# Kernel optimization log

Measured on AMD Instinct MI355X. Metric: run time of the kernel, lower is better.

Reference implementation:

```python
import jax, jax.numpy as jnp
import numpy as np

EPS = 1e-5

def _layernorm(x, g, b):
    m = jnp.mean(x, axis=-1, keepdims=True)
    v = jnp.mean(jnp.square(x - m), axis=-1, keepdims=True)
    return (x - m) * jax.lax.rsqrt(v + EPS) * g + b

def setup_inputs() -> dict:
    key = jax.random.key(0)
    B, S, D, H = 2, 2048, 1024, 16
    F = 4 * D
    ks = jax.random.split(key, 12)
    s = 1.0 / np.sqrt(D)
    inp = {
        "x": jax.random.normal(ks[0], (B, S, D), dtype=jnp.float32),
        "mask": jnp.ones((B, S), dtype=jnp.int32),
        "wq": jax.random.normal(ks[1], (D, D), dtype=jnp.float32) * s,
        "bq": jnp.zeros((D,), jnp.float32),
        "wk": jax.random.normal(ks[2], (D, D), dtype=jnp.float32) * s,
        "bk": jnp.zeros((D,), jnp.float32),
        "wv": jax.random.normal(ks[3], (D, D), dtype=jnp.float32) * s,
        "bv": jnp.zeros((D,), jnp.float32),
        "wo": jax.random.normal(ks[4], (D, D), dtype=jnp.float32) * s,
        "bo": jnp.zeros((D,), jnp.float32),
        "g1": jnp.ones((D,), jnp.float32),
        "be1": jnp.zeros((D,), jnp.float32),
        "g2": jnp.ones((D,), jnp.float32),
        "be2": jnp.zeros((D,), jnp.float32),
        "w1": jax.random.normal(ks[5], (D, F), dtype=jnp.float32) * s,
        "bf1": jnp.zeros((F,), jnp.float32),
        "w2": jax.random.normal(ks[6], (F, D), dtype=jnp.float32) * (1.0 / np.sqrt(F)),
        "bf2": jnp.zeros((D,), jnp.float32),
    }
    return inp

def reference(x, mask, wq, bq, wk, bk, wv, bv, wo, bo, g1, be1, g2, be2, w1, bf1, w2, bf2):
    B, S, D = x.shape
    H = 16
    hd = D // H
    residual = x
    xn = _layernorm(x, g1, be1)
    q = (xn @ wq + bq).reshape(B, S, H, hd).transpose(0, 2, 1, 3)  # [B,H,S,hd]
    k = (xn @ wk + bk).reshape(B, S, H, hd).transpose(0, 2, 1, 3)
    v = (xn @ wv + bv).reshape(B, S, H, hd).transpose(0, 2, 1, 3)
    scores = jnp.einsum('bhqd,bhkd->bhqk', q, k) / np.sqrt(hd)  # [B,H,S,S]
    scores = jnp.where(mask[:, None, None, :] == 0, jnp.float32(-1e9), scores)
    attn = jax.nn.softmax(scores, axis=-1)
    attended = jnp.einsum('bhqk,bhkd->bhqd', attn, v)
    attended = attended.transpose(0, 2, 1, 3).reshape(B, S, D)
    x = residual + (attended @ wo + bo)
    residual = x
    xn = _layernorm(x, g2, be2)
    ff = jax.nn.relu(xn @ w1 + bf1) @ w2 + bf2
    return residual + ff
```

## Files before the change

### kernel.cpp

```cpp
#include <hip/hip_runtime.h>
#include <hip/hip_bf16.h>


using bf16 = __hip_bfloat16;
typedef short bf16x8 __attribute__((ext_vector_type(8)));
typedef short bf16x4v __attribute__((ext_vector_type(4)));
typedef float f32x4 __attribute__((ext_vector_type(4)));

#if defined(__has_builtin)
#  if __has_builtin(__builtin_amdgcn_mfma_f32_16x16x16bf16_1k)
#    define HAVE_MFMA_K16 1
#  endif
#  if __has_builtin(__builtin_amdgcn_exp2f)
#    define EXP2F(x) __builtin_amdgcn_exp2f(x)
#  endif
#endif
#ifndef EXP2F
#  define EXP2F(x) __expf(0.6931471805599453f * (x))
#endif

__device__ __forceinline__ float toF(float v) { return v; }
__device__ __forceinline__ float toF(bf16 v) { return __bfloat162float(v); }
__device__ __forceinline__ void storeF(float* p, float v) { *p = v; }
__device__ __forceinline__ void storeF(bf16* p, float v) { *p = __float2bfloat16(v); }

__device__ __forceinline__ float waveReduceSum(float v) {
    #pragma unroll
    for (int o = 32; o > 0; o >>= 1) v += __shfl_down(v, o, 64);
    return v;
}

__device__ __forceinline__ void async16(const bf16* g, bf16* l) {
    __builtin_amdgcn_global_load_lds(
        (const __attribute__((address_space(1))) unsigned int*)g,
        (__attribute__((address_space(3))) unsigned int*)l,
        16, 0, 0);
}

__device__ __forceinline__ unsigned short bf16bits(float x) {
    union { bf16 h; unsigned short u; } e; e.h = __float2bfloat16(x);
    return e.u;
}

__global__ __launch_bounds__(256) void transpose_all(
        const float* __restrict__ wq, const float* __restrict__ wk,
        const float* __restrict__ wv, const float* __restrict__ wo,
        const float* __restrict__ w1, const float* __restrict__ w2,
        bf16* __restrict__ wqkvT, bf16* __restrict__ woT,
        bf16* __restrict__ w1T, bf16* __restrict__ w2T) {
    __shared__ float t[32][33];
    const int tI = blockIdx.x;
    const float* in; bf16* outT; int R, C, tl;
    if (tI < 4096) {
        const int seg = tI >> 10; tl = tI & 1023; R = 1024; C = 1024;
        in = (seg == 0) ? wq : (seg == 1) ? wk : (seg == 2) ? wv : wo;
        outT = (seg == 3) ? woT : wqkvT + (size_t)seg * 1024 * 1024;
    } else if (tI < 8192) {
        tl = tI - 4096; in = w1; outT = w1T; R = 1024; C = 4096;
    } else {
        tl = tI - 8192; in = w2; outT = w2T; R = 4096; C = 1024;
    }
    const int tc = C >> 5;
    const int c0 = (tl % tc) * 32, r0 = (tl / tc) * 32;
    const int lx = threadIdx.x & 31, ly = threadIdx.x >> 5;
    #pragma unroll
    for (int i = 0; i < 32; i += 8)
        t[ly + i][lx] = in[(size_t)(r0 + ly + i) * C + c0 + lx];
    __syncthreads();
    #pragma unroll
    for (int i = 0; i < 32; i += 8)
        outT[(size_t)(c0 + ly + i) * R + r0 + lx] = __float2bfloat16(t[lx][ly + i]);
}

template <typename InT>
__global__ __launch_bounds__(256) void ln_kernel(const InT* __restrict__ x,
                                                 const float* __restrict__ g,
                                                 const float* __restrict__ b,
                                                 bf16* __restrict__ out, int D) {
    const int row = blockIdx.x;
    const InT* xr = x + (size_t)row * D;
    float s = 0.f, s2 = 0.f;
    for (int i = threadIdx.x; i < D; i += 256) {
        float v = toF(xr[i]);
        s += v; s2 += v * v;
    }
    __shared__ float ws[4], ws2[4];
    int lane = threadIdx.x & 63, wid = threadIdx.x >> 6;
    s = waveReduceSum(s); s2 = waveReduceSum(s2);
    if (lane == 0) { ws[wid] = s; ws2[wid] = s2; }
    __syncthreads();
    float ts = ws[0] + ws[1] + ws[2] + ws[3];
    float ts2 = ws2[0] + ws2[1] + ws2[2] + ws2[3];
    float mean = ts / D;
    float var = ts2 / D - mean * mean;
    float rstd = rsqrtf(var + 1e-5f);
    bf16* outr = out + (size_t)row * D;
    for (int i = threadIdx.x; i < D; i += 256) {
        float v = (toF(xr[i]) - mean) * rstd * g[i] + b[i];
        outr[i] = __float2bfloat16(v);
    }
}

template <int BM, typename OutT, typename ResidT, bool RELU, bool HAS_RESID, bool BIAS3>
__global__ __launch_bounds__(256) void gemm_mfma(const bf16* __restrict__ A,
                                                 const bf16* __restrict__ BT,
                                                 const float* __restrict__ bias,
                                                 const float* __restrict__ biasK,
                                                 const float* __restrict__ biasV,
                                                 const ResidT* __restrict__ resid,
                                                 OutT* __restrict__ C,
                                                 int M, int N, int K) {
    constexpr int BK = 64;
    constexpr int MI = BM / 32;
    constexpr int AROWS = BM / 4;
    constexpr int ASEC = AROWS / 8;
    __shared__ bf16 As[BM][BK];
    __shared__ bf16 Bs[128][BK];
    const int tid = threadIdx.x, lane = tid & 63, wid = tid >> 6;
    const int m0 = blockIdx.y * BM, n0 = blockIdx.x * 128;
    const int wm = (BM == 128) ? (wid >> 1) * 64 : (wid & 1) * 32;
    const int wn = (BM == 128) ? (wid & 1) * 64 : (wid >> 1) * 64;

    f32x4 acc[MI][4] = {};

    const int srow = lane >> 3;
    const int scol = ((lane & 7) ^ srow) * 8;
    const bf16* Abase = A + (size_t)(m0 + wid * AROWS + srow) * K + scol;
    const bf16* Bbase = BT + (size_t)(n0 + wid * 32 + srow) * K + scol;

    const int fr = lane & 15;
    const int kg = lane >> 4;

    for (int k0 = 0; k0 < K; k0 += BK) {
        #pragma unroll
        for (int s = 0; s < ASEC; ++s)
            async16(Abase + (size_t)(s * 8) * K + k0, &As[wid * AROWS + s * 8][0]);
        #pragma unroll
        for (int s = 0; s < 4; ++s)
            async16(Bbase + (size_t)(s * 8) * K + k0, &Bs[wid * 32 + s * 8][0]);
        __syncthreads();

        #pragma unroll
        for (int ks = 0; ks < 2; ++ks) {
            const int pc = ((ks * 4 + kg) ^ (fr & 7)) * 16;
            bf16x8 aF[MI], bF[4];
            #pragma unroll
            for (int i = 0; i < MI; ++i)
                aF[i] = *(const bf16x8*)((const char*)&As[0][0]
                         + (size_t)(wm + i * 16 + fr) * 128 + pc);
            #pragma unroll
            for (int j = 0; j < 4; ++j)
                bF[j] = *(const bf16x8*)((const char*)&Bs[0][0]
                         + (size_t)(wn + j * 16 + fr) * 128 + pc);
            #pragma unroll
            for (int i = 0; i < MI; ++i)
                #pragma unroll
                for (int j = 0; j < 4; ++j)
                    acc[i][j] = __builtin_amdgcn_mfma_f32_16x16x32_bf16(
                        aF[i], bF[j], acc[i][j], 0, 0, 0);
        }
        __syncthreads();
    }

    const int col_l = lane & 15, row_l = (lane >> 4) * 4;
    #pragma unroll
    for (int j = 0; j < 4; ++j) {
        const int col = n0 + wn + j * 16 + col_l;
        float bvv;
        if (BIAS3) {
            const float* bp = (col < 1024) ? bias : ((col < 2048) ? biasK : biasV);
            bvv = bp[col & 1023];
        } else {
            bvv = bias[col];
        }
        #pragma unroll
        for (int i = 0; i < MI; ++i) {
            #pragma unroll
            for (int r = 0; r < 4; ++r) {
                const int row = m0 + wm + i * 16 + row_l + r;
                float v = acc[i][j][r] + bvv;
                if (RELU) v = fmaxf(v, 0.f);
                if (HAS_RESID) v += toF(resid[(size_t)row * N + col]);
                storeF(&C[(size_t)row * N + col], v);
            }
        }
    }
}

#if HAVE_MFMA_K16
__global__ __launch_bounds__(256) void attn_mfma(const bf16* __restrict__ qkv,
                                                 const int* __restrict__ mask,
                                                 bf16* __restrict__ outp,
                                                 int B, int S, int LD) {
    const int q0 = blockIdx.x * 128;
    const int h = blockIdx.y, b = blockIdx.z;
    const int Do = 1024;
    const int tid = threadIdx.x, lane = tid & 63, wid = tid >> 6;
    const int n = lane & 15, kg = lane >> 4;

    __shared__ bf16 Ks[64][66];
    __shared__ bf16 Vt[64][68];
    __shared__ float Mskf[64];

    const float QSCALE = 0.125f * 1.4426950408889634f;
    bf16x8 qf[2][2];
    #pragma unroll
    for (int u = 0; u < 2; ++u) {
        const bf16* qp = qkv + ((size_t)(b * S + q0 + wid * 32 + u * 16 + n)) * LD + h * 64 + kg * 8;
        union { uint4 uu; bf16x8 v; unsigned short s[8]; } c[2];
        c[0].uu = *(const uint4*)qp;
        c[1].uu = *(const uint4*)(qp + 32);
        #pragma unroll
        for (int t = 0; t < 2; ++t) {
            #pragma unroll
            for (int i = 0; i < 8; ++i) {
                union { float f; unsigned int u2; } d;
                d.u2 = ((unsigned int)c[t].s[i]) << 16;
                c[t].s[i] = bf16bits(d.f * QSCALE);
            }
            qf[u][t] = c[t].v;
        }
    }

    f32x4 acc[2][4] = {};
    float m[2] = {-1e30f, -1e30f}, l[2] = {0.f, 0.f};

    const int sr = tid >> 2, sc = (tid & 3) * 16;
    const int jp = tid & 31, dg = (tid >> 5) * 8;
    const bf16* kbase = qkv + (size_t)(b * S) * LD + 1024 + h * 64;
    const bf16* vbase = qkv + (size_t)(b * S) * LD + 2048 + h * 64;

    for (int j0 = 0; j0 < S; j0 += 64) {
        __syncthreads();
        {
            const bf16* kp = kbase + (size_t)(j0 + sr) * LD + sc;
            uint4 ka = *(const uint4*)kp;
            uint4 kc = *(const uint4*)(kp + 8);
            uint* kd = (uint*)((char*)&Ks[0][0] + sr * 132 + sc * 2);
            kd[0] = ka.x; kd[1] = ka.y; kd[2] = ka.z; kd[3] = ka.w;
            kd[4] = kc.x; kd[5] = kc.y; kd[6] = kc.z; kd[7] = kc.w;

            const bf16* vp = vbase + (size_t)(j0 + 2 * jp) * LD + dg;
            union { uint4 u; unsigned short s[8]; } va, vc;
            va.u = *(const uint4*)vp;
            vc.u = *(const uint4*)(vp + LD);
            #pragma unroll
            for (int i = 0; i < 8; ++i) {
                unsigned int pk = (unsigned int)va.s[i] | ((unsigned int)vc.s[i] << 16);
                *(unsigned int*)((char*)&Vt[0][0] + (size_t)(dg + i) * 136 + jp * 4) = pk;
            }
            if (tid < 64) Mskf[tid] = (mask[b * S + j0 + tid] == 0) ? -1e9f : 0.f;
        }
        __syncthreads();

        f32x4 st[2][4] = {};
        #pragma unroll
        for (int ks = 0; ks < 2; ++ks) {
            #pragma unroll
            for (int jt = 0; jt < 4; ++jt) {
                union { uint u[4]; bf16x8 v; } kf;
                const uint* bp = (const uint*)((const char*)&Ks[0][0]
                                 + (size_t)(jt * 16 + n) * 132 + ks * 64 + kg * 16);
                kf.u[0] = bp[0]; kf.u[1] = bp[1]; kf.u[2] = bp[2]; kf.u[3] = bp[3];
                st[0][jt] = __builtin_amdgcn_mfma_f32_16x16x32_bf16(kf.v, qf[0][ks], st[0][jt], 0, 0, 0);
                st[1][jt] = __builtin_amdgcn_mfma_f32_16x16x32_bf16(kf.v, qf[1][ks], st[1][jt], 0, 0, 0);
            }
        }

        bf16x4v pf[2][4];
        #pragma unroll
        for (int u = 0; u < 2; ++u) {
            float mx = m[u];
            #pragma unroll
            for (int jt = 0; jt < 4; ++jt) {
                f32x4 mb = *(const f32x4*)&Mskf[jt * 16 + kg * 4];
                #pragma unroll
                for (int r = 0; r < 4; ++r) {
                    st[u][jt][r] += mb[r];
                    mx = fmaxf(mx, st[u][jt][r]);
                }
            }
            mx = fmaxf(mx, __shfl_xor(mx, 16, 64));
            mx = fmaxf(mx, __shfl_xor(mx, 32, 64));
            float alpha = EXP2F(m[u] - mx);
            m[u] = mx;
            float ls = 0.f;
            #pragma unroll
            for (int jt = 0; jt < 4; ++jt) {
                union { unsigned short s[4]; bf16x4v v; } pk;
                #pragma unroll
                for (int r = 0; r < 4; ++r) {
                    union { float f; unsigned int u2; } p;
                    p.f = EXP2F(st[u][jt][r] - mx);
                    p.u2 &= 0xffff0000u;
                    ls += p.f;
                    pk.s[r] = (unsigned short)(p.u2 >> 16);
                }
                pf[u][jt] = pk.v;
            }
            ls += __shfl_xor(ls, 16, 64);
            ls += __shfl_xor(ls, 32, 64);
            l[u] = l[u] * alpha + ls;
            #pragma unroll
            for (int dt = 0; dt < 4; ++dt)
                #pragma unroll
                for (int r = 0; r < 4; ++r) acc[u][dt][r] *= alpha;
        }

        #pragma unroll
        for (int jt = 0; jt < 4; ++jt) {
            #pragma unroll
            for (int dt = 0; dt < 4; ++dt) {
                union { uint u[2]; bf16x4v v; } vf;
                const uint* vpp = (const uint*)((const char*)&Vt[0][0]
                                  + (size_t)(dt * 16 + n) * 136 + jt * 32 + kg * 8);
                vf.u[0] = vpp[0]; vf.u[1] = vpp[1];
                acc[0][dt] = __builtin_amdgcn_mfma_f32_16x16x16bf16_1k(vf.v, pf[0][jt], acc[0][dt], 0, 0, 0);
                acc[1][dt] = __builtin_amdgcn_mfma_f32_16x16x16bf16_1k(vf.v, pf[1][jt], acc[1][dt], 0, 0, 0);
            }
        }
    }

    #pragma unroll
    for (int u = 0; u < 2; ++u) {
        float inv = (l[u] > 0.f) ? (1.f / l[u]) : 0.f;
        bf16* op = outp + ((size_t)(b * S + q0 + wid * 32 + u * 16 + n)) * Do + h * 64;
        #pragma unroll
        for (int dt = 0; dt < 4; ++dt) {
            union { unsigned short s[4]; uint2 u2; } w;
            #pragma unroll
            for (int r = 0; r < 4; ++r) w.s[r] = bf16bits(acc[u][dt][r] * inv);
            *(uint2*)(op + dt * 16 + kg * 4) = w.u2;
        }
    }
}
#else
__global__ __launch_bounds__(256) void attn_mfma(const bf16* __restrict__ qkv,
                                                 const int* __restrict__ mask,
                                                 bf16* __restrict__ outp,
                                                 int B, int S, int LD) {
    const int h = blockIdx.y, b = blockIdx.z;
    const int Do = 1024;
    const int tid = threadIdx.x, lane = tid & 63, wid = tid >> 6;
    const int n = lane & 15, kg = lane >> 4;

    __shared__ bf16 Ks[64][66];
    __shared__ bf16 Vt[64][66];
    __shared__ bf16 Plds[4][16][66];
    __shared__ int  Msk[64];

    for (int half = 0; half < 2; ++half) {
        const int q0 = blockIdx.x * 128 + half * 64;
        __syncthreads();

        bf16x8 qf[2];
        {
            const bf16* qp = qkv + ((size_t)(b * S + q0 + wid * 16 + n)) * LD + h * 64 + kg * 8;
            union { uint4 u; bf16x8 v; } c0, c1;
            c0.u = *(const uint4*)qp;
            c1.u = *(const uint4*)(qp + 32);
            qf[0] = c0.v; qf[1] = c1.v;
        }

        f32x4 acc_o[4] = {};
        float m_r[4] = {-1e30f, -1e30f, -1e30f, -1e30f};
        float l_r[4] = {0.f, 0.f, 0.f, 0.f};

        const int sr = tid >> 2;
        const int sc = (tid & 3) * 16;
        const bf16* kbase = qkv + (size_t)(b * S) * LD + 1024 + h * 64;
        const bf16* vbase = qkv + (size_t)(b * S) * LD + 2048 + h * 64;

        for (int j0 = 0; j0 < S; j0 += 64) {
            __syncthreads();
            {
                const bf16* kp = kbase + (size_t)(j0 + sr) * LD + sc;
                uint4 ka = *(const uint4*)kp;
                uint4 kbv = *(const uint4*)(kp + 8);
                uint* kd = (uint*)((char*)&Ks[0][0] + sr * 132 + sc * 2);
                kd[0] = ka.x; kd[1] = ka.y; kd[2] = ka.z; kd[3] = ka.w;
                kd[4] = kbv.x; kd[5] = kbv.y; kd[6] = kbv.z; kd[7] = kbv.w;

                const bf16* vp = vbase + (size_t)(j0 + sr) * LD + sc;
                union { uint4 u[2]; unsigned short s[16]; } vv;
                vv.u[0] = *(const uint4*)vp;
                vv.u[1] = *(const uint4*)(vp + 8);
                #pragma unroll
                for (int i = 0; i < 16; ++i)
                    *((unsigned short*)((char*)&Vt[0][0] + (size_t)(sc + i) * 132 + sr * 2)) = vv.s[i];

                if (tid < 64) Msk[tid] = mask[b * S + j0 + tid];
            }
            __syncthreads();

            f32x4 st[4] = {};
            #pragma unroll
            for (int ks = 0; ks < 2; ++ks) {
                #pragma unroll
                for (int jt = 0; jt < 4; ++jt) {
                    union { uint u[4]; bf16x8 v; } bf;
                    const uint* bp = (const uint*)((const char*)&Ks[0][0]
                                     + (size_t)(jt * 16 + n) * 132 + ks * 64 + kg * 16);
                    bf.u[0] = bp[0]; bf.u[1] = bp[1]; bf.u[2] = bp[2]; bf.u[3] = bp[3];
                    st[jt] = __builtin_amdgcn_mfma_f32_16x16x32_bf16(qf[ks], bf.v, st[jt], 0, 0, 0);
                }
            }

            int mk[4];
            #pragma unroll
            for (int jt = 0; jt < 4; ++jt) mk[jt] = Msk[jt * 16 + n];

            #pragma unroll
            for (int r = 0; r < 4; ++r) {
                float mx = -1e30f;
                #pragma unroll
                for (int jt = 0; jt < 4; ++jt) {
                    float s = st[jt][r] * 0.125f;
                    if (mk[jt] == 0) s = -1e9f;
                    st[jt][r] = s;
                    mx = fmaxf(mx, s);
                }
                #pragma unroll
                for (int o = 1; o < 16; o <<= 1) mx = fmaxf(mx, __shfl_xor(mx, o, 64));
                float newm = fmaxf(m_r[r], mx);
                float alpha = __expf(m_r[r] - newm);
                m_r[r] = newm;
                float ls = 0.f;
                #pragma unroll
                for (int jt = 0; jt < 4; ++jt) {
                    float p = __expf(st[jt][r] - newm);
                    ls += p;
                    Plds[wid][kg * 4 + r][jt * 16 + n] = __float2bfloat16(p);
                }
                #pragma unroll
                for (int o = 1; o < 16; o <<= 1) ls += __shfl_xor(ls, o, 64);
                l_r[r] = l_r[r] * alpha + ls;
                #pragma unroll
                for (int dt = 0; dt < 4; ++dt) acc_o[dt][r] *= alpha;
            }

            __asm__ volatile("s_waitcnt lgkmcnt(0)" ::: "memory");

            #pragma unroll
            for (int ks = 0; ks < 2; ++ks) {
                union { uint u[4]; bf16x8 v; } af;
                const uint* ap = (const uint*)((const char*)&Plds[wid][0][0]
                                 + (size_t)n * 132 + ks * 64 + kg * 16);
                af.u[0] = ap[0]; af.u[1] = ap[1]; af.u[2] = ap[2]; af.u[3] = ap[3];
                #pragma unroll
                for (int dt = 0; dt < 4; ++dt) {
                    union { uint u[4]; bf16x8 v; } bf;
                    const uint* bp = (const uint*)((const char*)&Vt[0][0]
                                     + (size_t)(dt * 16 + n) * 132 + ks * 64 + kg * 16);
                    bf.u[0] = bp[0]; bf.u[1] = bp[1]; bf.u[2] = bp[2]; bf.u[3] = bp[3];
                    acc_o[dt] = __builtin_amdgcn_mfma_f32_16x16x32_bf16(af.v, bf.v, acc_o[dt], 0, 0, 0);
                }
            }
        }

        #pragma unroll
        for (int r = 0; r < 4; ++r) {
            float inv = (l_r[r] > 0.f) ? (1.f / l_r[r]) : 0.f;
            bf16* op = outp + ((size_t)(b * S + q0 + wid * 16 + kg * 4 + r)) * Do + h * 64 + n;
            #pragma unroll
            for (int dt = 0; dt < 4; ++dt)
                op[dt * 16] = __float2bfloat16(acc_o[dt][r] * inv);
        }
    }
}
#endif

extern "C" void kernel_launch(void* const* d_in, const int* in_sizes, int n_in,
                              void* d_out, int out_size, void* d_ws, size_t ws_size,
                              hipStream_t stream) {
    const int B = 2, S = 2048, D = 1024, H = 16, F = 4096;
    const int M = B * S;

    const float* x   = (const float*)d_in[0];
    const int*   mask= (const int*)  d_in[1];
    const float* wq  = (const float*)d_in[2];
    const float* bq  = (const float*)d_in[3];
    const float* wk  = (const float*)d_in[4];
    const float* bk  = (const float*)d_in[5];
    const float* wv  = (const float*)d_in[6];
    const float* bv  = (const float*)d_in[7];
    const float* wo  = (const float*)d_in[8];
    const float* bo  = (const float*)d_in[9];
    const float* g1  = (const float*)d_in[10];
    const float* be1 = (const float*)d_in[11];
    const float* g2  = (const float*)d_in[12];
    const float* be2 = (const float*)d_in[13];
    const float* w1  = (const float*)d_in[14];
    const float* bf1 = (const float*)d_in[15];
    const float* w2  = (const float*)d_in[16];
    const float* bf2 = (const float*)d_in[17];
    float* out = (float*)d_out;

    char* ws = (char*)d_ws;
    const size_t MB = 1024 * 1024;
    bf16* wqkvT = (bf16*)(ws + 0 * MB);
    bf16* woT   = (bf16*)(ws + 6 * MB);
    bf16* w1T   = (bf16*)(ws + 8 * MB);
    bf16* w2T   = (bf16*)(ws + 16 * MB);
    bf16* xn    = (bf16*)(ws + 24 * MB);
    bf16* qkv   = (bf16*)(ws + 32 * MB);
    bf16* att   = xn;

    const bool fullM = (ws_size >= 64 * MB);

    transpose_all<<<12288, 256, 0, stream>>>(wq, wk, wv, wo, w1, w2,
                                             wqkvT, woT, w1T, w2T);

    ln_kernel<float><<<M, 256, 0, stream>>>(x, g1, be1, xn, D);

    gemm_mfma<128, bf16, float, false, false, true><<<dim3(3072 / 128, M / 128), 256, 0, stream>>>(
        xn, wqkvT, bq, bk, bv, (const float*)nullptr, qkv, M, 3072, D);

    attn_mfma<<<dim3(S / 128, H, B), 256, 0, stream>>>(qkv, mask, att, B, S, 3072);

    gemm_mfma<64, float, float, false, true, false><<<dim3(D / 128, M / 64), 256, 0, stream>>>(
        att, woT, bo, nullptr, nullptr, x, out, M, D, D);

    if (fullM) {
        bf16* hid = (bf16*)(ws + 24 * MB);
        bf16* xn2 = (bf16*)(ws + 56 * MB);
        ln_kernel<float><<<M, 256, 0, stream>>>(out, g2, be2, xn2, D);
        gemm_mfma<128, bf16, float, true, false, false><<<dim3(F / 128, M / 128), 256, 0, stream>>>(
            xn2, w1T, bf1, nullptr, nullptr, (const float*)nullptr, hid, M, F, D);
        gemm_mfma<64, float, float, false, true, false><<<dim3(D / 128, M / 64), 256, 0, stream>>>(
            hid, w2T, bf2, nullptr, nullptr, out, out, M, D, F);
    } else {
        bf16* xn2 = (bf16*)(ws + 32 * MB);
        bf16* hid = (bf16*)(ws + 40 * MB);
        const int CH = 2048;
        ln_kernel<float><<<M, 256, 0, stream>>>(out, g2, be2, xn2, D);
        for (int c = 0; c < M / CH; ++c) {
            const size_t roff = (size_t)c * CH;
            gemm_mfma<128, bf16, float, true, false, false><<<dim3(F / 128, CH / 128), 256, 0, stream>>>(
                xn2 + roff * D, w1T, bf1, nullptr, nullptr, (const float*)nullptr, hid, CH, F, D);
            gemm_mfma<64, float, float, false, true, false><<<dim3(D / 128, CH / 64), 256, 0, stream>>>(
                hid, w2T, bf2, nullptr, nullptr, out + roff * D, out + roff * D, CH, D, F);
        }
    }
}
```

Before: 394.4 us.

## Halve attention query tile, skip mask add when unmasked, lazily rescale softmax

```diff
diff --git a/kernel.cpp b/kernel.cpp
--- a/kernel.cpp
+++ b/kernel.cpp
@@ -192,7 +192,7 @@
                                                  const int* __restrict__ mask,
                                                  bf16* __restrict__ outp,
                                                  int B, int S, int LD) {
-    const int q0 = blockIdx.x * 128;
+    const int q0 = blockIdx.x * 64;
     const int h = blockIdx.y, b = blockIdx.z;
     const int Do = 1024;
     const int tid = threadIdx.x, lane = tid & 63, wid = tid >> 6;
@@ -201,12 +201,12 @@
     __shared__ bf16 Ks[64][66];
     __shared__ bf16 Vt[64][68];
     __shared__ float Mskf[64];
+    __shared__ int sAny;
 
     const float QSCALE = 0.125f * 1.4426950408889634f;
-    bf16x8 qf[2][2];
-    #pragma unroll
-    for (int u = 0; u < 2; ++u) {
-        const bf16* qp = qkv + ((size_t)(b * S + q0 + wid * 32 + u * 16 + n)) * LD + h * 64 + kg * 8;
+    bf16x8 qf[2];
+    {
+        const bf16* qp = qkv + ((size_t)(b * S + q0 + wid * 16 + n)) * LD + h * 64 + kg * 8;
         union { uint4 uu; bf16x8 v; unsigned short s[8]; } c[2];
         c[0].uu = *(const uint4*)qp;
         c[1].uu = *(const uint4*)(qp + 32);
@@ -218,12 +218,12 @@
                 d.u2 = ((unsigned int)c[t].s[i]) << 16;
                 c[t].s[i] = bf16bits(d.f * QSCALE);
             }
-            qf[u][t] = c[t].v;
-        }
-    }
-
-    f32x4 acc[2][4] = {};
-    float m[2] = {-1e30f, -1e30f}, l[2] = {0.f, 0.f};
+            qf[t] = c[t].v;
+        }
+    }
+
+    f32x4 acc[4] = {};
+    float m = -1e30f, l = 0.f;
 
     const int sr = tid >> 2, sc = (tid & 3) * 16;
     const int jp = tid & 31, dg = (tid >> 5) * 8;
@@ -249,11 +249,16 @@
                 unsigned int pk = (unsigned int)va.s[i] | ((unsigned int)vc.s[i] << 16);
                 *(unsigned int*)((char*)&Vt[0][0] + (size_t)(dg + i) * 136 + jp * 4) = pk;
             }
-            if (tid < 64) Mskf[tid] = (mask[b * S + j0 + tid] == 0) ? -1e9f : 0.f;
+            if (tid < 64) {
+                int mz = (mask[b * S + j0 + tid] == 0);
+                Mskf[tid] = mz ? -1e9f : 0.f;
+                unsigned long long bl = __ballot(mz);
+                if (tid == 0) sAny = (bl != 0ull) ? 1 : 0;
+            }
         }
         __syncthreads();
 
-        f32x4 st[2][4] = {};
+        f32x4 st[4] = {};
         #pragma unroll
         for (int ks = 0; ks < 2; ++ks) {
             #pragma unroll
@@ -262,50 +267,56 @@
                 const uint* bp = (const uint*)((const char*)&Ks[0][0]
                                  + (size_t)(jt * 16 + n) * 132 + ks * 64 + kg * 16);
                 kf.u[0] = bp[0]; kf.u[1] = bp[1]; kf.u[2] = bp[2]; kf.u[3] = bp[3];
-                st[0][jt] = __builtin_amdgcn_mfma_f32_16x16x32_bf16(kf.v, qf[0][ks], st[0][jt], 0, 0, 0);
-                st[1][jt] = __builtin_amdgcn_mfma_f32_16x16x32_bf16(kf.v, qf[1][ks], st[1][jt], 0, 0, 0);
-            }
-        }
-
-        bf16x4v pf[2][4];
-        #pragma unroll
-        for (int u = 0; u < 2; ++u) {
-            float mx = m[u];
+                st[jt] = __builtin_amdgcn_mfma_f32_16x16x32_bf16(kf.v, qf[ks], st[jt], 0, 0, 0);
+            }
+        }
+
+        if (sAny) {
             #pragma unroll
             for (int jt = 0; jt < 4; ++jt) {
                 f32x4 mb = *(const f32x4*)&Mskf[jt * 16 + kg * 4];
                 #pragma unroll
-                for (int r = 0; r < 4; ++r) {
-                    st[u][jt][r] += mb[r];
-                    mx = fmaxf(mx, st[u][jt][r]);
-                }
-            }
-            mx = fmaxf(mx, __shfl_xor(mx, 16, 64));
-            mx = fmaxf(mx, __shfl_xor(mx, 32, 64));
-            float alpha = EXP2F(m[u] - mx);
-            m[u] = mx;
-            float ls = 0.f;
-            #pragma unroll
-            for (int jt = 0; jt < 4; ++jt) {
-                union { unsigned short s[4]; bf16x4v v; } pk;
-                #pragma unroll
-                for (int r = 0; r < 4; ++r) {
-                    union { float f; unsigned int u2; } p;
-                    p.f = EXP2F(st[u][jt][r] - mx);
-                    p.u2 &= 0xffff0000u;
-                    ls += p.f;
-                    pk.s[r] = (unsigned short)(p.u2 >> 16);
-                }
-                pf[u][jt] = pk.v;
-            }
-            ls += __shfl_xor(ls, 16, 64);
-            ls += __shfl_xor(ls, 32, 64);
-            l[u] = l[u] * alpha + ls;
+                for (int r = 0; r < 4; ++r) st[jt][r] += mb[r];
+            }
+        }
+
+        float mx = st[0][0];
+        #pragma unroll
+        for (int jt = 0; jt < 4; ++jt)
+            #pragma unroll
+            for (int r = 0; r < 4; ++r) mx = fmaxf(mx, st[jt][r]);
+        mx = fmaxf(mx, __shfl_xor(mx, 16, 64));
+        mx = fmaxf(mx, __shfl_xor(mx, 32, 64));
+
+        if (__any(mx > m + 8.f)) {
+            float newm = fmaxf(m, mx);
+            float alpha = EXP2F(m - newm);
+            m = newm;
+            l *= alpha;
             #pragma unroll
             for (int dt = 0; dt < 4; ++dt)
                 #pragma unroll
-                for (int r = 0; r < 4; ++r) acc[u][dt][r] *= alpha;
-        }
+                for (int r = 0; r < 4; ++r) acc[dt][r] *= alpha;
+        }
+
+        bf16x4v pf[4];
+        float ls = 0.f;
+        #pragma unroll
+        for (int jt = 0; jt < 4; ++jt) {
+            union { unsigned short s[4]; bf16x4v v; } pk;
+            #pragma unroll
+            for (int r = 0; r < 4; ++r) {
+                union { float f; unsigned int u2; } p;
+                p.f = EXP2F(st[jt][r] - m);
+                p.u2 &= 0xffff0000u;
+                ls += p.f;
+                pk.s[r] = (unsigned short)(p.u2 >> 16);
+            }
+            pf[jt] = pk.v;
+        }
+        ls += __shfl_xor(ls, 16, 64);
+        ls += __shfl_xor(ls, 32, 64);
+        l += ls;
 
         #pragma unroll
         for (int jt = 0; jt < 4; ++jt) {
@@ -315,23 +326,19 @@
                 const uint* vpp = (const uint*)((const char*)&Vt[0][0]
                                   + (size_t)(dt * 16 + n) * 136 + jt * 32 + kg * 8);
                 vf.u[0] = vpp[0]; vf.u[1] = vpp[1];
-                acc[0][dt] = __builtin_amdgcn_mfma_f32_16x16x16bf16_1k(vf.v, pf[0][jt], acc[0][dt], 0, 0, 0);
-                acc[1][dt] = __builtin_amdgcn_mfma_f32_16x16x16bf16_1k(vf.v, pf[1][jt], acc[1][dt], 0, 0, 0);
-            }
-        }
-    }
-
+                acc[dt] = __builtin_amdgcn_mfma_f32_16x16x16bf16_1k(vf.v, pf[jt], acc[dt], 0, 0, 0);
+            }
+        }
+    }
+
+    float inv = (l > 0.f) ? (1.f / l) : 0.f;
+    bf16* op = outp + ((size_t)(b * S + q0 + wid * 16 + n)) * Do + h * 64;
     #pragma unroll
-    for (int u = 0; u < 2; ++u) {
-        float inv = (l[u] > 0.f) ? (1.f / l[u]) : 0.f;
-        bf16* op = outp + ((size_t)(b * S + q0 + wid * 32 + u * 16 + n)) * Do + h * 64;
-        #pragma unroll
-        for (int dt = 0; dt < 4; ++dt) {
-            union { unsigned short s[4]; uint2 u2; } w;
-            #pragma unroll
-            for (int r = 0; r < 4; ++r) w.s[r] = bf16bits(acc[u][dt][r] * inv);
-            *(uint2*)(op + dt * 16 + kg * 4) = w.u2;
-        }
+    for (int dt = 0; dt < 4; ++dt) {
+        union { unsigned short s[4]; uint2 u2; } w;
+        #pragma unroll
+        for (int r = 0; r < 4; ++r) w.s[r] = bf16bits(acc[dt][r] * inv);
+        *(uint2*)(op + dt * 16 + kg * 4) = w.u2;
     }
 }
 #else
@@ -349,8 +356,8 @@
     __shared__ bf16 Plds[4][16][66];
     __shared__ int  Msk[64];
 
-    for (int half = 0; half < 2; ++half) {
-        const int q0 = blockIdx.x * 128 + half * 64;
+    for (int half = 0; half < 1; ++half) {
+        const int q0 = blockIdx.x * 64;
         __syncthreads();
 
         bf16x8 qf[2];
@@ -516,7 +523,7 @@
     gemm_mfma<128, bf16, float, false, false, true><<<dim3(3072 / 128, M / 128), 256, 0, stream>>>(
         xn, wqkvT, bq, bk, bv, (const float*)nullptr, qkv, M, 3072, D);
 
-    attn_mfma<<<dim3(S / 128, H, B), 256, 0, stream>>>(qkv, mask, att, B, S, 3072);
+    attn_mfma<<<dim3(S / 64, H, B), 256, 0, stream>>>(qkv, mask, att, B, S, 3072);
 
     gemm_mfma<64, float, float, false, true, false><<<dim3(D / 128, M / 64), 256, 0, stream>>>(
         att, woT, bo, nullptr, nullptr, x, out, M, D, D);
```

Result: slower. 403.2 us (+2.2%).

## Double-buffer K/V tiles in attention and use lazy softmax rescaling

Applied to the files above, without the earlier changes.

```diff
diff --git a/kernel.cpp b/kernel.cpp
--- a/kernel.cpp
+++ b/kernel.cpp
@@ -198,9 +198,10 @@
     const int tid = threadIdx.x, lane = tid & 63, wid = tid >> 6;
     const int n = lane & 15, kg = lane >> 4;
 
-    __shared__ bf16 Ks[64][66];
-    __shared__ bf16 Vt[64][68];
-    __shared__ float Mskf[64];
+    __shared__ bf16 Ks[2][64][66];
+    __shared__ bf16 Vt[2][64][68];
+    __shared__ float Mskf[2][64];
+    __shared__ int sAny[2];
 
     const float QSCALE = 0.125f * 1.4426950408889634f;
     bf16x8 qf[2][2];
@@ -230,28 +231,53 @@
     const bf16* kbase = qkv + (size_t)(b * S) * LD + 1024 + h * 64;
     const bf16* vbase = qkv + (size_t)(b * S) * LD + 2048 + h * 64;
 
-    for (int j0 = 0; j0 < S; j0 += 64) {
-        __syncthreads();
+    uint4 ka, kc, vau, vcu;
+    int mz = 0;
+
+    {
+        const bf16* kp = kbase + (size_t)sr * LD + sc;
+        ka = *(const uint4*)kp;
+        kc = *(const uint4*)(kp + 8);
+        const bf16* vp = vbase + (size_t)(2 * jp) * LD + dg;
+        vau = *(const uint4*)vp;
+        vcu = *(const uint4*)(vp + LD);
+        if (tid < 64) mz = (mask[b * S + tid] == 0);
+    }
+
+    const int NT = S / 64;
+    for (int t = 0; t < NT; ++t) {
+        const int cur = t & 1;
+
         {
-            const bf16* kp = kbase + (size_t)(j0 + sr) * LD + sc;
-            uint4 ka = *(const uint4*)kp;
-            uint4 kc = *(const uint4*)(kp + 8);
-            uint* kd = (uint*)((char*)&Ks[0][0] + sr * 132 + sc * 2);
+            uint* kd = (uint*)((char*)&Ks[cur][0][0] + sr * 132 + sc * 2);
             kd[0] = ka.x; kd[1] = ka.y; kd[2] = ka.z; kd[3] = ka.w;
             kd[4] = kc.x; kd[5] = kc.y; kd[6] = kc.z; kd[7] = kc.w;
 
-            const bf16* vp = vbase + (size_t)(j0 + 2 * jp) * LD + dg;
-            union { uint4 u; unsigned short s[8]; } va, vc;
-            va.u = *(const uint4*)vp;
-            vc.u = *(const uint4*)(vp + LD);
+            union { uint4 u4; unsigned short s[8]; } va, vc;
+            va.u4 = vau; vc.u4 = vcu;
             #pragma unroll
             for (int i = 0; i < 8; ++i) {
                 unsigned int pk = (unsigned int)va.s[i] | ((unsigned int)vc.s[i] << 16);
-                *(unsigned int*)((char*)&Vt[0][0] + (size_t)(dg + i) * 136 + jp * 4) = pk;
-            }
-            if (tid < 64) Mskf[tid] = (mask[b * S + j0 + tid] == 0) ? -1e9f : 0.f;
+                *(unsigned int*)((char*)&Vt[cur][0][0] + (size_t)(dg + i) * 136 + jp * 4) = pk;
+            }
+            if (tid < 64) {
+                Mskf[cur][tid] = mz ? -1e9f : 0.f;
+                unsigned long long bl = __ballot(mz);
+                if (tid == 0) sAny[cur] = (bl != 0ull) ? 1 : 0;
+            }
         }
         __syncthreads();
+
+        if (t + 1 < NT) {
+            const int j0 = (t + 1) * 64;
+            const bf16* kp = kbase + (size_t)(j0 + sr) * LD + sc;
+            ka = *(const uint4*)kp;
+            kc = *(const uint4*)(kp + 8);
+            const bf16* vp = vbase + (size_t)(j0 + 2 * jp) * LD + dg;
+            vau = *(const uint4*)vp;
+            vcu = *(const uint4*)(vp + LD);
+            if (tid < 64) mz = (mask[b * S + j0 + tid] == 0);
+        }
 
         f32x4 st[2][4] = {};
         #pragma unroll
@@ -259,7 +285,7 @@
             #pragma unroll
             for (int jt = 0; jt < 4; ++jt) {
                 union { uint u[4]; bf16x8 v; } kf;
-                const uint* bp = (const uint*)((const char*)&Ks[0][0]
+                const uint* bp = (const uint*)((const char*)&Ks[cur][0][0]
                                  + (size_t)(jt * 16 + n) * 132 + ks * 64 + kg * 16);
                 kf.u[0] = bp[0]; kf.u[1] = bp[1]; kf.u[2] = bp[2]; kf.u[3] = bp[3];
                 st[0][jt] = __builtin_amdgcn_mfma_f32_16x16x32_bf16(kf.v, qf[0][ks], st[0][jt], 0, 0, 0);
@@ -267,23 +293,50 @@
             }
         }
 
+        if (sAny[cur]) {
+            #pragma unroll
+            for (int u = 0; u < 2; ++u) {
+                #pragma unroll
+                for (int jt = 0; jt < 4; ++jt) {
+                    f32x4 mb = *(const f32x4*)&Mskf[cur][jt * 16 + kg * 4];
+                    #pragma unroll
+                    for (int r = 0; r < 4; ++r) st[u][jt][r] += mb[r];
+                }
+            }
+        }
+
+        float mx0 = st[0][0][0], mx1 = st[1][0][0];
+        #pragma unroll
+        for (int jt = 0; jt < 4; ++jt) {
+            #pragma unroll
+            for (int r = 0; r < 4; ++r) {
+                mx0 = fmaxf(mx0, st[0][jt][r]);
+                mx1 = fmaxf(mx1, st[1][jt][r]);
+            }
+        }
+        mx0 = fmaxf(mx0, __shfl_xor(mx0, 16, 64));
+        mx0 = fmaxf(mx0, __shfl_xor(mx0, 32, 64));
+        mx1 = fmaxf(mx1, __shfl_xor(mx1, 16, 64));
+        mx1 = fmaxf(mx1, __shfl_xor(mx1, 32, 64));
+
+        if (__any((mx0 > m[0] + 8.f) || (mx1 > m[1] + 8.f))) {
+            float mxa[2] = {mx0, mx1};
+            #pragma unroll
+            for (int u = 0; u < 2; ++u) {
+                float newm = fmaxf(m[u], mxa[u]);
+                float alpha = EXP2F(m[u] - newm);
+                m[u] = newm;
+                l[u] *= alpha;
+                #pragma unroll
+                for (int dt = 0; dt < 4; ++dt)
+                    #pragma unroll
+                    for (int r = 0; r < 4; ++r) acc[u][dt][r] *= alpha;
+            }
+        }
+
         bf16x4v pf[2][4];
         #pragma unroll
         for (int u = 0; u < 2; ++u) {
-            float mx = m[u];
-            #pragma unroll
-            for (int jt = 0; jt < 4; ++jt) {
-                f32x4 mb = *(const f32x4*)&Mskf[jt * 16 + kg * 4];
-                #pragma unroll
-                for (int r = 0; r < 4; ++r) {
-                    st[u][jt][r] += mb[r];
-                    mx = fmaxf(mx, st[u][jt][r]);
-                }
-            }
-            mx = fmaxf(mx, __shfl_xor(mx, 16, 64));
-            mx = fmaxf(mx, __shfl_xor(mx, 32, 64));
-            float alpha = EXP2F(m[u] - mx);
-            m[u] = mx;
             float ls = 0.f;
             #pragma unroll
             for (int jt = 0; jt < 4; ++jt) {
@@ -291,7 +344,7 @@
                 #pragma unroll
                 for (int r = 0; r < 4; ++r) {
                     union { float f; unsigned int u2; } p;
-                    p.f = EXP2F(st[u][jt][r] - mx);
+                    p.f = EXP2F(st[u][jt][r] - m[u]);
                     p.u2 &= 0xffff0000u;
                     ls += p.f;
                     pk.s[r] = (unsigned short)(p.u2 >> 16);
@@ -300,11 +353,7 @@
             }
             ls += __shfl_xor(ls, 16, 64);
             ls += __shfl_xor(ls, 32, 64);
-            l[u] = l[u] * alpha + ls;
-            #pragma unroll
-            for (int dt = 0; dt < 4; ++dt)
-                #pragma unroll
-                for (int r = 0; r < 4; ++r) acc[u][dt][r] *= alpha;
+            l[u] += ls;
         }
 
         #pragma unroll
@@ -312,7 +361,7 @@
             #pragma unroll
             for (int dt = 0; dt < 4; ++dt) {
                 union { uint u[2]; bf16x4v v; } vf;
-                const uint* vpp = (const uint*)((const char*)&Vt[0][0]
+                const uint* vpp = (const uint*)((const char*)&Vt[cur][0][0]
                                   + (size_t)(dt * 16 + n) * 136 + jt * 32 + kg * 8);
                 vf.u[0] = vpp[0]; vf.u[1] = vpp[1];
                 acc[0][dt] = __builtin_amdgcn_mfma_f32_16x16x16bf16_1k(vf.v, pf[0][jt], acc[0][dt], 0, 0, 0);
```

Measured after the change: 392.2 us. About the same (-0.6%).
